# Optimization experiments

Measured on AMD Instinct MI355X. Metric: run time of the kernel, lower is better.

## Reference

```python
import jax, jax.numpy as jnp
import numpy as np

B, S, H = 4, 2048, 1024
NH, HD = 16, 64
SCALE = float(np.sqrt(HD))


def setup_inputs() -> dict:
    key = jax.random.key(0)
    ks = jax.random.split(key, 6)
    std = 1.0 / np.sqrt(H)
    return {
        "x": jax.random.normal(ks[0], (B, S, H), dtype=jnp.float32),
        "mask": jnp.ones((B, S), dtype=jnp.int32),
        "Wq": jax.random.normal(ks[1], (H, H), dtype=jnp.float32) * std,
        "bq": jnp.zeros((H,), dtype=jnp.float32),
        "Wk": jax.random.normal(ks[2], (H, H), dtype=jnp.float32) * std,
        "bk": jnp.zeros((H,), dtype=jnp.float32),
        "Wv": jax.random.normal(ks[3], (H, H), dtype=jnp.float32) * std,
        "bv": jnp.zeros((H,), dtype=jnp.float32),
        "Wo": jax.random.normal(ks[4], (H, H), dtype=jnp.float32) * std,
        "bo": jnp.zeros((H,), dtype=jnp.float32),
    }


def reference(x, mask, Wq, bq, Wk, bk, Wv, bv, Wo, bo):
    b, s, h = x.shape
    # QKV projections (torch Linear: x @ W.T + b), split into heads: [b, nh, s, hd]
    def proj(W, bias):
        return (x @ W.T + bias).reshape(b, s, NH, HD).transpose(0, 2, 1, 3)
    Q, K, V = proj(Wq, bq), proj(Wk, bk), proj(Wv, bv)
    scores = jnp.einsum("bnqd,bnkd->bnqk", Q, K) / SCALE  # [b, nh, s, s]
    # mask: [b, s] -> [b, 1, 1, s]; masked positions -> -inf
    m = mask[:, None, None, :]
    scores = jnp.where(m == 0, -jnp.inf, scores)
    attn = jax.nn.softmax(scores, axis=-1)
    attn = jnp.nan_to_num(attn, nan=0.0)  # rows fully masked -> 0
    # dropout is identity in eval mode
    ctx = jnp.einsum("bnqk,bnkd->bnqd", attn, V)
    ctx = ctx.transpose(0, 2, 1, 3).reshape(b, s, h)
    return ctx @ Wo.T + bo
```

## Files before the change

kernel.cpp:

```cpp
#include <hip/hip_runtime.h>
#include <hip/hip_bf16.h>

#define NB    4
#define NS    2048
#define NHID  1024
#define NHEADS 16
#define DHEAD 64
#define M_TOT (NB * NS)

using b8    = __attribute__((ext_vector_type(8))) __bf16;
using f32x4 = __attribute__((ext_vector_type(4))) float;

static __device__ inline f32x4 mfma16(b8 a, b8 b, f32x4 c) {
    return __builtin_amdgcn_mfma_f32_16x16x32_bf16(a, b, c, 0, 0, 0);
}

static __device__ inline void gload16(const __bf16* g, __bf16* l) {
    __builtin_amdgcn_global_load_lds((const __attribute__((address_space(1))) void*)g,
                                     (__attribute__((address_space(3))) void*)l,
                                     16, 0, 0);
}

__global__ __launch_bounds__(256) void cvt_x(const float* __restrict__ in,
                                             __bf16* __restrict__ out, int n4) {
    int idx = blockIdx.x * 256 + threadIdx.x;
    if (idx < n4) {
        float4 v = ((const float4*)in)[idx];
        union { __bf16 h[4]; short4 s; } u;
        u.h[0] = (__bf16)v.x; u.h[1] = (__bf16)v.y;
        u.h[2] = (__bf16)v.z; u.h[3] = (__bf16)v.w;
        ((short4*)out)[idx] = u.s;
    }
}

__global__ __launch_bounds__(256) void cvt_w4(const float* __restrict__ w0,
                                              const float* __restrict__ w1,
                                              const float* __restrict__ w2,
                                              const float* __restrict__ w3,
                                              __bf16* __restrict__ out) {
    const int n4 = NHID * NHID / 4;
    const float* w = (blockIdx.y == 0) ? w0 : (blockIdx.y == 1) ? w1
                   : (blockIdx.y == 2) ? w2 : w3;
    __bf16* o = out + (size_t)blockIdx.y * NHID * NHID;
    int idx = blockIdx.x * 256 + threadIdx.x;
    if (idx < n4) {
        float4 v = ((const float4*)w)[idx];
        union { __bf16 h[4]; short4 s; } u;
        u.h[0] = (__bf16)v.x; u.h[1] = (__bf16)v.y;
        u.h[2] = (__bf16)v.z; u.h[3] = (__bf16)v.w;
        ((short4*)o)[idx] = u.s;
    }
}

#define GEMM_CORE_BK64(A_, W_, m0_, n0_)                                        \
    __shared__ __bf16 la[2 * 128 * 32];                                         \
    __shared__ __bf16 lb[2 * 128 * 32];                                         \
    const int t    = threadIdx.x;                                               \
    const int w    = t >> 6;                                                    \
    const int lane = t & 63;                                                    \
    const int g    = lane >> 4, i = lane & 15;                                  \
    const int rowS = t >> 2;                                                    \
    const int kcol = (t & 3) * 8;                                               \
    const __bf16* gA[4]; const __bf16* gB[4];                                   \
    _Pragma("unroll")                                                           \
    for (int j = 0; j < 4; ++j) {                                               \
        const int rr = (j & 1) * 64 + rowS;                                     \
        const int kk = (j >> 1) * 32 + kcol;                                    \
        gA[j] = (A_) + (size_t)((m0_) + rr) * NHID + kk;                        \
        gB[j] = (W_) + (size_t)((n0_) + rr) * NHID + kk;                        \
    }                                                                           \
    __bf16* lAd[4]; __bf16* lBd[4];                                             \
    _Pragma("unroll")                                                           \
    for (int j = 0; j < 4; ++j) {                                               \
        lAd[j] = la + j * 2048 + w * 512;                                       \
        lBd[j] = lb + j * 2048 + w * 512;                                       \
    }                                                                           \
    const int wm = w >> 1, wn = w & 1;                                          \
    f32x4 acc[4][4] = {};                                                       \
    for (int kt = 0; kt < NHID / 64; ++kt) {                                    \
        const int koff = kt * 64;                                               \
        _Pragma("unroll")                                                       \
        for (int j = 0; j < 4; ++j) gload16(gA[j] + koff, lAd[j]);              \
        _Pragma("unroll")                                                       \
        for (int j = 0; j < 4; ++j) gload16(gB[j] + koff, lBd[j]);              \
        __syncthreads();                                                        \
        _Pragma("unroll")                                                       \
        for (int h = 0; h < 2; ++h) {                                           \
            b8 af[4], bf[4];                                                    \
            _Pragma("unroll")                                                   \
            for (int jm = 0; jm < 4; ++jm)                                      \
                af[jm] = *(const b8*)(la + h * 4096 +                           \
                                      (wm * 64 + jm * 16 + i) * 32 + g * 8);    \
            _Pragma("unroll")                                                   \
            for (int jn = 0; jn < 4; ++jn)                                      \
                bf[jn] = *(const b8*)(lb + h * 4096 +                           \
                                      (wn * 64 + jn * 16 + i) * 32 + g * 8);    \
            _Pragma("unroll")                                                   \
            for (int jm = 0; jm < 4; ++jm)                                      \
                _Pragma("unroll")                                               \
                for (int jn = 0; jn < 4; ++jn)                                  \
                    acc[jm][jn] = mfma16(af[jm], bf[jn], acc[jm][jn]);          \
        }                                                                       \
        __syncthreads();                                                        \
    }

__global__ __launch_bounds__(256) void gemm_qkv(
    const __bf16* __restrict__ A,
    const __bf16* __restrict__ W,
    const float*  __restrict__ bq,
    const float*  __restrict__ bk,
    const float*  __restrict__ bv,
    __bf16* __restrict__ q_out,
    __bf16* __restrict__ k_out,
    __bf16* __restrict__ vt_out)
{
    const int lin = blockIdx.y * 24 + blockIdx.x;
    const int xcd = lin & 7;
    const int jj  = lin >> 3;
    const int bx  = jj >> 3;
    const int byl = jj & 7;
    const int n0  = bx * 128;
    const int m0  = (xcd * 8 + byl) * 128;
    const int which = n0 >> 10;
    const int n_loc = n0 & (NHID - 1);

    GEMM_CORE_BK64(A, W, m0, n0)

    const float* bias = (which == 0) ? bq : (which == 1) ? bk : bv;
    float bvv[4];
#pragma unroll
    for (int jn = 0; jn < 4; ++jn) bvv[jn] = bias[n_loc + wn * 64 + jn * 16 + i];

    const int nh = (n_loc + wn * 64) >> 6;
    if (which < 2) {
        __bf16* out = (which == 0) ? q_out : k_out;
#pragma unroll
        for (int jm = 0; jm < 4; ++jm)
#pragma unroll
            for (int r = 0; r < 4; ++r) {
                int m = m0 + wm * 64 + jm * 16 + g * 4 + r;
                int b_idx = m >> 11, s = m & (NS - 1);
                __bf16* orow = out + (((size_t)(b_idx * NHEADS + nh)) * NS + s) * DHEAD + i;
#pragma unroll
                for (int jn = 0; jn < 4; ++jn)
                    orow[jn * 16] = (__bf16)(acc[jm][jn][r] + bvv[jn]);
            }
    } else {
#pragma unroll
        for (int jm = 0; jm < 4; ++jm) {
            int sbase = m0 + wm * 64 + jm * 16 + g * 4;
            int b_idx = sbase >> 11, s = sbase & (NS - 1);
#pragma unroll
            for (int jn = 0; jn < 4; ++jn) {
                int hd = jn * 16 + i;
                union { __bf16 h[4]; ushort4 u; } pk;
#pragma unroll
                for (int r = 0; r < 4; ++r)
                    pk.h[r] = (__bf16)(acc[jm][jn][r] + bvv[jn]);
                __bf16* op = vt_out + (((size_t)(b_idx * NHEADS + nh)) * DHEAD + hd) * NS + s;
                *(ushort4*)op = pk.u;
            }
        }
    }
}

__global__ __launch_bounds__(256) void gemm_out(
    const __bf16* __restrict__ A,
    const __bf16* __restrict__ W,
    const float*  __restrict__ bias,
    float* __restrict__ out)
{
    const int lin = blockIdx.y * 8 + blockIdx.x;
    const int xcd = lin & 7;
    const int jj  = lin >> 3;
    const int bx  = jj >> 3;
    const int byl = jj & 7;
    const int n0  = bx * 128;
    const int m0  = (xcd * 8 + byl) * 128;

    GEMM_CORE_BK64(A, W, m0, n0)

    float bvv[4];
#pragma unroll
    for (int jn = 0; jn < 4; ++jn) bvv[jn] = bias[n0 + wn * 64 + jn * 16 + i];

#pragma unroll
    for (int jm = 0; jm < 4; ++jm)
#pragma unroll
        for (int r = 0; r < 4; ++r) {
            int m = m0 + wm * 64 + jm * 16 + g * 4 + r;
            float* orow = out + (size_t)m * NHID + n0 + wn * 64 + i;
#pragma unroll
            for (int jn = 0; jn < 4; ++jn)
                orow[jn * 16] = acc[jm][jn][r] + bvv[jn];
        }
}

#define PPITCH 72

__global__ __launch_bounds__(256, 4) void attn_kernel(
    const __bf16* __restrict__ q_ws,
    const __bf16* __restrict__ k_ws,
    const __bf16* __restrict__ vt_ws,
    const int*    __restrict__ mask,
    __bf16* __restrict__ ctx)
{
    __shared__ __bf16 lk[64 * 64];
    __shared__ __bf16 lv[64 * 64];
    __shared__ __bf16 lp[4][2][16 * PPITCH];

    const int t    = threadIdx.x;
    const int lane = t & 63;
    const int wv   = t >> 6;
    const int g = lane >> 4, i = lane & 15;

    const int lin  = blockIdx.y * 16 + blockIdx.x;
    const int xcd  = lin & 7;
    const int jj   = lin >> 3;
    const int bh   = xcd * 8 + (jj >> 4);
    const int qb   = jj & 15;
    const int b_idx = bh >> 4;
    const int nh    = bh & 15;
    const int qbase = qb * 128 + wv * 32;

    const float C1 = 0.125f * 1.44269504f;
    const float C2 = 20.0f * 1.44269504f;

    union { ushort u[8]; b8 v; } ones_u;
#pragma unroll
    for (int j = 0; j < 8; ++j) ones_u.u[j] = 0x3F80;
    const b8 ones = ones_u.v;

    const __bf16* Kbase = k_ws  + (size_t)bh * NS * DHEAD;
    const __bf16* Vtb   = vt_ws + (size_t)bh * DHEAD * NS;
    const int*    mrow  = mask  + b_idx * NS;

    const __bf16* kSrc[2];
    const __bf16* vSrc[2];
#pragma unroll
    for (int j = 0; j < 2; ++j) {
        int d   = j * 256 + t;
        int row = d >> 3;
        int hc  = (d & 7) ^ (row & 7);
        kSrc[j] = Kbase + (size_t)row * DHEAD + hc * 8;
        vSrc[j] = Vtb   + (size_t)row * NS   + hc * 8;
    }
    __bf16* lkW[2] = { lk + wv * 512, lk + 2048 + wv * 512 };
    __bf16* lvW[2] = { lv + wv * 512, lv + 2048 + wv * 512 };

    b8 qa[2][2];
#pragma unroll
    for (int st = 0; st < 2; ++st) {
        const __bf16* Qp = q_ws + ((size_t)bh * NS + qbase + st * 16 + i) * DHEAD;
        qa[st][0] = *(const b8*)(Qp + g * 8);
        qa[st][1] = *(const b8*)(Qp + 32 + g * 8);
    }

    f32x4 o[2][4] = {};
    f32x4 ol[2]   = {};

    const int ix = i & 7;

    for (int kt = 0; kt < NS / 64; ++kt) {
        const int k0 = kt * 64;

        gload16(kSrc[0] + (size_t)k0 * DHEAD, lkW[0]);
        gload16(kSrc[1] + (size_t)k0 * DHEAD, lkW[1]);
        gload16(vSrc[0] + k0,                 lvW[0]);
        gload16(vSrc[1] + k0,                 lvW[1]);
        __syncthreads();

        f32x4 s[2][4];
#pragma unroll
        for (int st = 0; st < 2; ++st)
#pragma unroll
            for (int kc = 0; kc < 4; ++kc)
                s[st][kc] = (f32x4){0.f, 0.f, 0.f, 0.f};
#pragma unroll
        for (int kc = 0; kc < 4; ++kc) {
            const int keyl = kc * 16 + i;
            b8 kb0 = *(const b8*)(lk + ((size_t)keyl * 8 + ((0 * 4 + g) ^ ix)) * 8);
            b8 kb1 = *(const b8*)(lk + ((size_t)keyl * 8 + ((1 * 4 + g) ^ ix)) * 8);
#pragma unroll
            for (int st = 0; st < 2; ++st) {
                s[st][kc] = mfma16(qa[st][0], kb0, s[st][kc]);
                s[st][kc] = mfma16(qa[st][1], kb1, s[st][kc]);
            }
        }

        float mf[4];
#pragma unroll
        for (int kc = 0; kc < 4; ++kc) mf[kc] = mrow[k0 + kc * 16 + i] ? 1.f : 0.f;
#pragma unroll
        for (int st = 0; st < 2; ++st) {
            __bf16* ldsw = lp[wv][st];
#pragma unroll
            for (int kc = 0; kc < 4; ++kc)
#pragma unroll
                for (int r = 0; r < 4; ++r) {
                    float p = __builtin_amdgcn_exp2f(s[st][kc][r] * C1 - C2) * mf[kc];
                    ldsw[(g * 4 + r) * PPITCH + kc * 16 + i] = (__bf16)p;
                }
        }
        __asm__ volatile("" ::: "memory");

#pragma unroll
        for (int c = 0; c < 2; ++c) {
            b8 pa0 = *(const b8*)(lp[wv][0] + i * PPITCH + c * 32 + g * 8);
            b8 pa1 = *(const b8*)(lp[wv][1] + i * PPITCH + c * 32 + g * 8);
#pragma unroll
            for (int hc = 0; hc < 4; ++hc) {
                const int hdl = hc * 16 + i;
                b8 vb = *(const b8*)(lv + ((size_t)hdl * 8 + ((c * 4 + g) ^ ix)) * 8);
                o[0][hc] = mfma16(pa0, vb, o[0][hc]);
                o[1][hc] = mfma16(pa1, vb, o[1][hc]);
            }
            ol[0] = mfma16(pa0, ones, ol[0]);
            ol[1] = mfma16(pa1, ones, ol[1]);
        }
        __syncthreads();
    }

#pragma unroll
    for (int st = 0; st < 2; ++st)
#pragma unroll
        for (int r = 0; r < 4; ++r) {
            float l = ol[st][r];
            float inv = l > 0.f ? 1.0f / l : 0.f;
            int srow = qbase + st * 16 + g * 4 + r;
            __bf16* op = ctx + ((size_t)b_idx * NS + srow) * NHID + nh * DHEAD;
            op[i]      = (__bf16)(o[st][0][r] * inv);
            op[16 + i] = (__bf16)(o[st][1][r] * inv);
            op[32 + i] = (__bf16)(o[st][2][r] * inv);
            op[48 + i] = (__bf16)(o[st][3][r] * inv);
        }
}

extern "C" void kernel_launch(void* const* d_in, const int* in_sizes, int n_in,
                              void* d_out, int out_size, void* d_ws, size_t ws_size,
                              hipStream_t stream) {
    const float* x    = (const float*)d_in[0];
    const int*   mask = (const int*)  d_in[1];
    const float* Wq   = (const float*)d_in[2];
    const float* bq   = (const float*)d_in[3];
    const float* Wk   = (const float*)d_in[4];
    const float* bk   = (const float*)d_in[5];
    const float* Wv   = (const float*)d_in[6];
    const float* bv   = (const float*)d_in[7];
    const float* Wo   = (const float*)d_in[8];
    const float* bo   = (const float*)d_in[9];
    float* out = (float*)d_out;

    const size_t elems = (size_t)M_TOT * NHID;
    __bf16* q_ws   = (__bf16*)d_ws;
    __bf16* k_ws   = q_ws  + elems;
    __bf16* vt_ws  = k_ws  + elems;
    __bf16* ctx_ws = vt_ws + elems;
    __bf16* w_bf16 = ctx_ws + elems;
    __bf16* x_bf16 = ctx_ws;

    dim3 blk(256);

    cvt_x<<<dim3((elems / 4 + 255) / 256), blk, 0, stream>>>(x, x_bf16, (int)(elems / 4));
    cvt_w4<<<dim3(NHID * NHID / 4 / 256, 4), blk, 0, stream>>>(Wq, Wk, Wv, Wo, w_bf16);

    const size_t wsz = (size_t)NHID * NHID;

    dim3 qkv_grid(3 * NHID / 128, M_TOT / 128);
    gemm_qkv<<<qkv_grid, blk, 0, stream>>>(x_bf16, w_bf16, bq, bk, bv,
                                           q_ws, k_ws, vt_ws);

    dim3 attn_grid(NS / 128, NB * NHEADS);
    attn_kernel<<<attn_grid, blk, 0, stream>>>(q_ws, k_ws, vt_ws, mask, ctx_ws);

    dim3 out_grid(NHID / 128, M_TOT / 128);
    gemm_out<<<out_grid, blk, 0, stream>>>(ctx_ws, w_bf16 + 3 * wsz, bo, out);
}
```

Baseline: 292.4 us.

## Switch attention to 32x32x16 MFMA with transposed scores and register-shuffled P

Rewrites the attention inner loop to use 32x32x16 bf16 MFMA, computing S^T = K·Q^T so each lane holds a query column. The probability tile is repacked into B operands via cross-half lane shuffles instead of a round trip through LDS, which frees the P scratch buffer. The mask is now read as int4 vectors, and the output goes through a swizzled LDS staging buffer so each lane can store one 16-byte row chunk. The K/V LDS swizzle is also changed to reduce bank conflicts, at the cost of extra shuffle and select instructions.

Result: slower. 319.1 us (+9.1%).

```diff
diff --git a/kernel.cpp b/kernel.cpp
--- a/kernel.cpp
+++ b/kernel.cpp
@@ -8,11 +8,21 @@
 #define DHEAD 64
 #define M_TOT (NB * NS)
 
-using b8    = __attribute__((ext_vector_type(8))) __bf16;
-using f32x4 = __attribute__((ext_vector_type(4))) float;
+using b8     = __attribute__((ext_vector_type(8))) __bf16;
+using f32x4  = __attribute__((ext_vector_type(4))) float;
+using f32x16 = __attribute__((ext_vector_type(16))) float;
 
 static __device__ inline f32x4 mfma16(b8 a, b8 b, f32x4 c) {
     return __builtin_amdgcn_mfma_f32_16x16x32_bf16(a, b, c, 0, 0, 0);
+}
+static __device__ inline f32x16 mfma32(b8 a, b8 b, f32x16 c) {
+    return __builtin_amdgcn_mfma_f32_32x32x16_bf16(a, b, c, 0, 0, 0);
+}
+static __device__ inline f32x16 zero16() {
+    f32x16 v;
+#pragma unroll
+    for (int k = 0; k < 16; ++k) v[k] = 0.f;
+    return v;
 }
 
 static __device__ inline void gload16(const __bf16* g, __bf16* l) {
@@ -20,6 +30,8 @@
                                      (__attribute__((address_space(3))) void*)l,
                                      16, 0, 0);
 }
+
+#define SWZK(row) ((((row) ^ ((row) >> 3))) & 7)
 
 __global__ __launch_bounds__(256) void cvt_x(const float* __restrict__ in,
                                              __bf16* __restrict__ out, int n4) {
@@ -196,8 +208,6 @@
         }
 }
 
-#define PPITCH 72
-
 __global__ __launch_bounds__(256, 4) void attn_kernel(
     const __bf16* __restrict__ q_ws,
     const __bf16* __restrict__ k_ws,
@@ -205,14 +215,15 @@
     const int*    __restrict__ mask,
     __bf16* __restrict__ ctx)
 {
-    __shared__ __bf16 lk[64 * 64];
-    __shared__ __bf16 lv[64 * 64];
-    __shared__ __bf16 lp[4][2][16 * PPITCH];
+    __shared__ __bf16 lds[8192];
+    __bf16* lk = lds;
+    __bf16* lv = lds + 4096;
 
     const int t    = threadIdx.x;
     const int lane = t & 63;
     const int wv   = t >> 6;
-    const int g = lane >> 4, i = lane & 15;
+    const int h    = lane >> 5;
+    const int c    = lane & 31;
 
     const int lin  = blockIdx.y * 16 + blockIdx.x;
     const int xcd  = lin & 7;
@@ -241,25 +252,21 @@
     for (int j = 0; j < 2; ++j) {
         int d   = j * 256 + t;
         int row = d >> 3;
-        int hc  = (d & 7) ^ (row & 7);
+        int hc  = (d & 7) ^ SWZK(row);
         kSrc[j] = Kbase + (size_t)row * DHEAD + hc * 8;
         vSrc[j] = Vtb   + (size_t)row * NS   + hc * 8;
     }
     __bf16* lkW[2] = { lk + wv * 512, lk + 2048 + wv * 512 };
     __bf16* lvW[2] = { lv + wv * 512, lv + 2048 + wv * 512 };
 
-    b8 qa[2][2];
-#pragma unroll
-    for (int st = 0; st < 2; ++st) {
-        const __bf16* Qp = q_ws + ((size_t)bh * NS + qbase + st * 16 + i) * DHEAD;
-        qa[st][0] = *(const b8*)(Qp + g * 8);
-        qa[st][1] = *(const b8*)(Qp + 32 + g * 8);
-    }
-
-    f32x4 o[2][4] = {};
-    f32x4 ol[2]   = {};
-
-    const int ix = i & 7;
+    b8 qbf[4];
+    {
+        const __bf16* Qp = q_ws + ((size_t)bh * NS + qbase + c) * DHEAD + h * 8;
+#pragma unroll
+        for (int hh = 0; hh < 4; ++hh) qbf[hh] = *(const b8*)(Qp + hh * 16);
+    }
+
+    f32x16 oacc0 = zero16(), oacc1 = zero16(), lacc = zero16();
 
     for (int kt = 0; kt < NS / 64; ++kt) {
         const int k0 = kt * 64;
@@ -270,70 +277,83 @@
         gload16(vSrc[1] + k0,                 lvW[1]);
         __syncthreads();
 
-        f32x4 s[2][4];
-#pragma unroll
-        for (int st = 0; st < 2; ++st)
-#pragma unroll
-            for (int kc = 0; kc < 4; ++kc)
-                s[st][kc] = (f32x4){0.f, 0.f, 0.f, 0.f};
-#pragma unroll
-        for (int kc = 0; kc < 4; ++kc) {
-            const int keyl = kc * 16 + i;
-            b8 kb0 = *(const b8*)(lk + ((size_t)keyl * 8 + ((0 * 4 + g) ^ ix)) * 8);
-            b8 kb1 = *(const b8*)(lk + ((size_t)keyl * 8 + ((1 * 4 + g) ^ ix)) * 8);
-#pragma unroll
-            for (int st = 0; st < 2; ++st) {
-                s[st][kc] = mfma16(qa[st][0], kb0, s[st][kc]);
-                s[st][kc] = mfma16(qa[st][1], kb1, s[st][kc]);
-            }
-        }
-
-        float mf[4];
-#pragma unroll
-        for (int kc = 0; kc < 4; ++kc) mf[kc] = mrow[k0 + kc * 16 + i] ? 1.f : 0.f;
-#pragma unroll
-        for (int st = 0; st < 2; ++st) {
-            __bf16* ldsw = lp[wv][st];
-#pragma unroll
-            for (int kc = 0; kc < 4; ++kc)
-#pragma unroll
-                for (int r = 0; r < 4; ++r) {
-                    float p = __builtin_amdgcn_exp2f(s[st][kc][r] * C1 - C2) * mf[kc];
-                    ldsw[(g * 4 + r) * PPITCH + kc * 16 + i] = (__bf16)p;
-                }
-        }
-        __asm__ volatile("" ::: "memory");
-
-#pragma unroll
-        for (int c = 0; c < 2; ++c) {
-            b8 pa0 = *(const b8*)(lp[wv][0] + i * PPITCH + c * 32 + g * 8);
-            b8 pa1 = *(const b8*)(lp[wv][1] + i * PPITCH + c * 32 + g * 8);
-#pragma unroll
-            for (int hc = 0; hc < 4; ++hc) {
-                const int hdl = hc * 16 + i;
-                b8 vb = *(const b8*)(lv + ((size_t)hdl * 8 + ((c * 4 + g) ^ ix)) * 8);
-                o[0][hc] = mfma16(pa0, vb, o[0][hc]);
-                o[1][hc] = mfma16(pa1, vb, o[1][hc]);
-            }
-            ol[0] = mfma16(pa0, ones, ol[0]);
-            ol[1] = mfma16(pa1, ones, ol[1]);
+#pragma unroll
+        for (int sb = 0; sb < 2; ++sb) {
+            f32x16 st = zero16();
+            const int krow = sb * 32 + c;
+            const int ks   = SWZK(krow);
+#pragma unroll
+            for (int hh = 0; hh < 4; ++hh) {
+                b8 ka = *(const b8*)(lk + krow * 64 + ((2 * hh + h) ^ ks) * 8);
+                st = mfma32(ka, qbf[hh], st);
+            }
+
+            int dw[8];
+#pragma unroll
+            for (int q = 0; q < 4; ++q) {
+                const int4 mm = *(const int4*)(mrow + k0 + sb * 32 + q * 8 + h * 4);
+                float p0 = mm.x ? __builtin_amdgcn_exp2f(st[q*4+0] * C1 - C2) : 0.f;
+                float p1 = mm.y ? __builtin_amdgcn_exp2f(st[q*4+1] * C1 - C2) : 0.f;
+                float p2 = mm.z ? __builtin_amdgcn_exp2f(st[q*4+2] * C1 - C2) : 0.f;
+                float p3 = mm.w ? __builtin_amdgcn_exp2f(st[q*4+3] * C1 - C2) : 0.f;
+                union { __bf16 b[2]; int u; } pk;
+                pk.b[0] = (__bf16)p0; pk.b[1] = (__bf16)p1; dw[q*2]   = pk.u;
+                pk.b[0] = (__bf16)p2; pk.b[1] = (__bf16)p3; dw[q*2+1] = pk.u;
+            }
+            int x[8];
+#pragma unroll
+            for (int e = 0; e < 8; ++e) x[e] = __shfl_xor(dw[e], 32, 64);
+            union { int u[4]; b8 v; } pb0u, pb1u;
+            if (h == 0) {
+                pb0u.u[0] = dw[0]; pb0u.u[1] = dw[1]; pb0u.u[2] = x[0];  pb0u.u[3] = x[1];
+                pb1u.u[0] = dw[4]; pb1u.u[1] = dw[5]; pb1u.u[2] = x[4];  pb1u.u[3] = x[5];
+            } else {
+                pb0u.u[0] = x[2];  pb0u.u[1] = x[3];  pb0u.u[2] = dw[2]; pb0u.u[3] = dw[3];
+                pb1u.u[0] = x[6];  pb1u.u[1] = x[7];  pb1u.u[2] = dw[6]; pb1u.u[3] = dw[7];
+            }
+            const b8 pb0 = pb0u.v, pb1 = pb1u.v;
+
+            {
+                const int vrow = c;
+                const int vs   = SWZK(vrow);
+                b8 va0 = *(const b8*)(lv + vrow * 64 + ((sb * 4 + 0 + h) ^ vs) * 8);
+                b8 va1 = *(const b8*)(lv + vrow * 64 + ((sb * 4 + 2 + h) ^ vs) * 8);
+                oacc0 = mfma32(va0, pb0, oacc0);
+                oacc0 = mfma32(va1, pb1, oacc0);
+            }
+            {
+                const int vrow = 32 + c;
+                const int vs   = SWZK(vrow);
+                b8 va0 = *(const b8*)(lv + vrow * 64 + ((sb * 4 + 0 + h) ^ vs) * 8);
+                b8 va1 = *(const b8*)(lv + vrow * 64 + ((sb * 4 + 2 + h) ^ vs) * 8);
+                oacc1 = mfma32(va0, pb0, oacc1);
+                oacc1 = mfma32(va1, pb1, oacc1);
+            }
+            lacc = mfma32(ones, pb0, lacc);
+            lacc = mfma32(ones, pb1, lacc);
         }
         __syncthreads();
     }
 
-#pragma unroll
-    for (int st = 0; st < 2; ++st)
-#pragma unroll
-        for (int r = 0; r < 4; ++r) {
-            float l = ol[st][r];
-            float inv = l > 0.f ? 1.0f / l : 0.f;
-            int srow = qbase + st * 16 + g * 4 + r;
-            __bf16* op = ctx + ((size_t)b_idx * NS + srow) * NHID + nh * DHEAD;
-            op[i]      = (__bf16)(o[st][0][r] * inv);
-            op[16 + i] = (__bf16)(o[st][1][r] * inv);
-            op[32 + i] = (__bf16)(o[st][2][r] * inv);
-            op[48 + i] = (__bf16)(o[st][3][r] * inv);
+    const float lsum = lacc[0];
+    const float inv  = lsum > 0.f ? 1.0f / lsum : 0.f;
+    __bf16* scr = lds + wv * 2048;
+#pragma unroll
+    for (int tl = 0; tl < 2; ++tl)
+#pragma unroll
+        for (int r = 0; r < 16; ++r) {
+            const int hd  = (r & 3) + 8 * (r >> 2) + 4 * h + 32 * tl;
+            const float v = (tl == 0 ? oacc0[r] : oacc1[r]) * inv;
+            scr[c * 64 + (((hd >> 3) ^ SWZK(c)) * 8) + (hd & 7)] = (__bf16)v;
         }
+    __asm__ volatile("" ::: "memory");
+#pragma unroll
+    for (int j = 0; j < 4; ++j) {
+        const int c8 = h * 4 + j;
+        b8 row = *(const b8*)(scr + c * 64 + ((c8 ^ SWZK(c)) * 8));
+        __bf16* op = ctx + ((size_t)b_idx * NS + qbase + c) * NHID + nh * 64 + c8 * 8;
+        *(b8*)op = row;
+    }
 }
 
 extern "C" void kernel_launch(void* const* d_in, const int* in_sizes, int n_in,
```
